# Kernel optimization log

Hardware: AMD Instinct MI355X
Metric: run time of the kernel (lower is better)

Reference implementation:

```python
import jax, jax.numpy as jnp
import numpy as np


def setup_inputs() -> dict:
    key = jax.random.key(0)
    k1, k2 = jax.random.split(key)
    user_attributes = jax.random.normal(k1, (32, 128, 256), dtype=jnp.float32)
    image_attributes = jax.random.normal(k2, (32, 256, 256), dtype=jnp.float32)
    return {"user_attributes": user_attributes, "image_attributes": image_attributes}


def reference(user_attributes, image_attributes):
    # Math: inter[b,u,i,d] = user[b,u,d] * img[b,i,d]
    #   sum over i -> user[b,u,d] * sum_i img[b,i,d]
    #   sum over u -> img[b,i,d]  * sum_u user[b,u,d]
    # Algebraically identical to the O(U*I*D) broadcast, without materializing it.
    img_sum = jnp.sum(image_attributes, axis=1, keepdims=True)   # [B,1,D]
    user_sum = jnp.sum(user_attributes, axis=1, keepdims=True)   # [B,1,D]
    aggregated_interactions_user = user_attributes * img_sum     # [B,U,D]
    aggregated_interactions_img = image_attributes * user_sum    # [B,I,D]
    return (aggregated_interactions_user, aggregated_interactions_img)
```

## Files before the change

kernel.cpp:

```cpp
#include <hip/hip_runtime.h>

#define B 32
#define U 128
#define I 256
#define D 256

#define PU_OFF 0
#define PI_OFF (B * 4 * D)

__global__ void __launch_bounds__(256) reduce_partial_kernel(
    const float* __restrict__ user,
    const float* __restrict__ img,
    float* __restrict__ ws) {
  __shared__ float4 part[4][64];
  const int blk  = blockIdx.x;
  const int tid  = threadIdx.x;
  const int rg   = tid >> 6;
  const int lane = tid & 63;

  const float4* src4;
  float4* dst4;
  if (blk < 128) {
    const int b = blk >> 2, c = blk & 3;
    src4 = (const float4*)(user + (size_t)b * U * D) + (size_t)c * 32 * 64;
    dst4 = (float4*)(ws + PU_OFF) + (size_t)(b * 4 + c) * 64;
  } else {
    const int k = blk - 128;
    const int b = k >> 3, c = k & 7;
    src4 = (const float4*)(img + (size_t)b * I * D) + (size_t)c * 32 * 64;
    dst4 = (float4*)(ws + PI_OFF) + (size_t)(b * 8 + c) * 64;
  }

  float4 acc = make_float4(0.f, 0.f, 0.f, 0.f);
  #pragma unroll
  for (int it = 0; it < 8; ++it) {
    const float4 v = src4[(size_t)(rg * 8 + it) * 64 + lane];
    acc.x += v.x; acc.y += v.y; acc.z += v.z; acc.w += v.w;
  }
  part[rg][lane] = acc;
  __syncthreads();
  if (rg == 0) {
    const float4 a = part[0][lane];
    const float4 b4 = part[1][lane];
    const float4 c = part[2][lane];
    const float4 e = part[3][lane];
    dst4[lane] = make_float4(a.x + b4.x + c.x + e.x,
                             a.y + b4.y + c.y + e.y,
                             a.z + b4.z + c.z + e.z,
                             a.w + b4.w + c.w + e.w);
  }
}

__global__ void __launch_bounds__(256) multiply_kernel(
    const float* __restrict__ user,
    const float* __restrict__ img,
    const float* __restrict__ ws,
    float* __restrict__ out) {
  constexpr int U4  = U * D / 4;
  constexpr int I4  = I * D / 4;
  constexpr int NU4 = B * U4;
  constexpr int NI4 = B * I4;

  const int g = blockIdx.x * blockDim.x + threadIdx.x;
  const float4* u4  = (const float4*)user;
  const float4* i4  = (const float4*)img;
  const float4* pu4 = (const float4*)(ws + PU_OFF);
  const float4* pi4 = (const float4*)(ws + PI_OFF);
  float4* o4 = (float4*)out;

  if (g < NU4) {
    const int b  = g >> 13;
    const int d4 = g & 63;
    const float4* p = pi4 + (size_t)b * 8 * 64 + d4;
    float4 s = p[0];
    #pragma unroll
    for (int c = 1; c < 8; ++c) {
      const float4 t = p[(size_t)c * 64];
      s.x += t.x; s.y += t.y; s.z += t.z; s.w += t.w;
    }
    const float4 v = u4[g];
    o4[g] = make_float4(v.x * s.x, v.y * s.y, v.z * s.z, v.w * s.w);
  } else if (g < NU4 + NI4) {
    const int k  = g - NU4;
    const int b  = k >> 14;
    const int d4 = k & 63;
    const float4* p = pu4 + (size_t)b * 4 * 64 + d4;
    float4 s = p[0];
    #pragma unroll
    for (int c = 1; c < 4; ++c) {
      const float4 t = p[(size_t)c * 64];
      s.x += t.x; s.y += t.y; s.z += t.z; s.w += t.w;
    }
    const float4 v = i4[k];
    o4[NU4 + k] = make_float4(v.x * s.x, v.y * s.y, v.z * s.z, v.w * s.w);
  }
}

extern "C" void kernel_launch(void* const* d_in, const int* in_sizes, int n_in,
                              void* d_out, int out_size, void* d_ws, size_t ws_size,
                              hipStream_t stream) {
  const float* user = (const float*)d_in[0];
  const float* img  = (const float*)d_in[1];
  float* out = (float*)d_out;
  float* ws  = (float*)d_ws;

  reduce_partial_kernel<<<dim3(384), dim3(256), 0, stream>>>(user, img, ws);

  constexpr int total4 = (B * U * D + B * I * D) / 4;
  multiply_kernel<<<dim3(total4 / 256), dim3(256), 0, stream>>>(user, img, ws, out);
}
```

Measured before the change: 71.16 us.

## Fuse column-sum reduction and scaling into a single kernel with redundant reductions

Replaces the two-kernel pipeline (partial reductions to workspace, then an elementwise multiply) with one kernel. Each block recomputes the full column sum of the opposite tensor for its batch and then scales its own 32-row slice. This removes one launch, the workspace round trip and the dependency between kernels. The cost is redundant reads: each img batch is summed by 4 blocks and each user batch by 8, roughly doubling total input reads, though some of those may hit in cache.

```diff
diff --git a/kernel.cpp b/kernel.cpp
--- a/kernel.cpp
+++ b/kernel.cpp
@@ -4,95 +4,78 @@
 #define U 128
 #define I 256
 #define D 256
+#define D4 (D / 4)
 
-#define PU_OFF 0
-#define PI_OFF (B * 4 * D)
-
-__global__ void __launch_bounds__(256) reduce_partial_kernel(
+__global__ void __launch_bounds__(256) fused_interaction_kernel(
     const float* __restrict__ user,
     const float* __restrict__ img,
-    float* __restrict__ ws) {
+    float* __restrict__ out) {
   __shared__ float4 part[4][64];
-  const int blk  = blockIdx.x;
-  const int tid  = threadIdx.x;
-  const int rg   = tid >> 6;
-  const int lane = tid & 63;
+  const int tid = threadIdx.x;
+  const int rg  = tid >> 6;
+  const int d4  = tid & 63;
+  const int blk = blockIdx.x;
 
-  const float4* src4;
-  float4* dst4;
+  const float4* u4 = (const float4*)user;
+  const float4* i4 = (const float4*)img;
+  float4* o4 = (float4*)out;
+  constexpr size_t NU4 = (size_t)B * U * D4;
+
   if (blk < 128) {
     const int b = blk >> 2, c = blk & 3;
-    src4 = (const float4*)(user + (size_t)b * U * D) + (size_t)c * 32 * 64;
-    dst4 = (float4*)(ws + PU_OFF) + (size_t)(b * 4 + c) * 64;
+    const float4* ib = i4 + (size_t)b * I * D4;
+
+    float4 acc = make_float4(0.f, 0.f, 0.f, 0.f);
+    #pragma unroll 8
+    for (int t = 0; t < 64; ++t) {
+      const float4 v = ib[(size_t)(rg + 4 * t) * D4 + d4];
+      acc.x += v.x; acc.y += v.y; acc.z += v.z; acc.w += v.w;
+    }
+    part[rg][d4] = acc;
+    __syncthreads();
+    const float4 s0 = part[0][d4], s1 = part[1][d4];
+    const float4 s2 = part[2][d4], s3 = part[3][d4];
+    const float4 s = make_float4(s0.x + s1.x + s2.x + s3.x,
+                                 s0.y + s1.y + s2.y + s3.y,
+                                 s0.z + s1.z + s2.z + s3.z,
+                                 s0.w + s1.w + s2.w + s3.w);
+
+    const float4* ub = u4 + (size_t)b * U * D4;
+    float4* ob = o4 + (size_t)b * U * D4;
+    #pragma unroll
+    for (int it = 0; it < 8; ++it) {
+      const size_t r = (size_t)(c * 32 + rg * 8 + it);
+      const float4 v = ub[r * D4 + d4];
+      ob[r * D4 + d4] = make_float4(v.x * s.x, v.y * s.y, v.z * s.z, v.w * s.w);
+    }
   } else {
     const int k = blk - 128;
     const int b = k >> 3, c = k & 7;
-    src4 = (const float4*)(img + (size_t)b * I * D) + (size_t)c * 32 * 64;
-    dst4 = (float4*)(ws + PI_OFF) + (size_t)(b * 8 + c) * 64;
-  }
+    const float4* ub = u4 + (size_t)b * U * D4;
 
-  float4 acc = make_float4(0.f, 0.f, 0.f, 0.f);
-  #pragma unroll
-  for (int it = 0; it < 8; ++it) {
-    const float4 v = src4[(size_t)(rg * 8 + it) * 64 + lane];
-    acc.x += v.x; acc.y += v.y; acc.z += v.z; acc.w += v.w;
-  }
-  part[rg][lane] = acc;
-  __syncthreads();
-  if (rg == 0) {
-    const float4 a = part[0][lane];
-    const float4 b4 = part[1][lane];
-    const float4 c = part[2][lane];
-    const float4 e = part[3][lane];
-    dst4[lane] = make_float4(a.x + b4.x + c.x + e.x,
-                             a.y + b4.y + c.y + e.y,
-                             a.z + b4.z + c.z + e.z,
-                             a.w + b4.w + c.w + e.w);
-  }
-}
+    float4 acc = make_float4(0.f, 0.f, 0.f, 0.f);
+    #pragma unroll 8
+    for (int t = 0; t < 32; ++t) {
+      const float4 v = ub[(size_t)(rg + 4 * t) * D4 + d4];
+      acc.x += v.x; acc.y += v.y; acc.z += v.z; acc.w += v.w;
+    }
+    part[rg][d4] = acc;
+    __syncthreads();
+    const float4 s0 = part[0][d4], s1 = part[1][d4];
+    const float4 s2 = part[2][d4], s3 = part[3][d4];
+    const float4 s = make_float4(s0.x + s1.x + s2.x + s3.x,
+                                 s0.y + s1.y + s2.y + s3.y,
+                                 s0.z + s1.z + s2.z + s3.z,
+                                 s0.w + s1.w + s2.w + s3.w);
 
-__global__ void __launch_bounds__(256) multiply_kernel(
-    const float* __restrict__ user,
-    const float* __restrict__ img,
-    const float* __restrict__ ws,
-    float* __restrict__ out) {
-  constexpr int U4  = U * D / 4;
-  constexpr int I4  = I * D / 4;
-  constexpr int NU4 = B * U4;
-  constexpr int NI4 = B * I4;
-
-  const int g = blockIdx.x * blockDim.x + threadIdx.x;
-  const float4* u4  = (const float4*)user;
-  const float4* i4  = (const float4*)img;
-  const float4* pu4 = (const float4*)(ws + PU_OFF);
-  const float4* pi4 = (const float4*)(ws + PI_OFF);
-  float4* o4 = (float4*)out;
-
-  if (g < NU4) {
-    const int b  = g >> 13;
-    const int d4 = g & 63;
-    const float4* p = pi4 + (size_t)b * 8 * 64 + d4;
-    float4 s = p[0];
+    const float4* ib = i4 + (size_t)b * I * D4;
+    float4* ob = o4 + NU4 + (size_t)b * I * D4;
     #pragma unroll
-    for (int c = 1; c < 8; ++c) {
-      const float4 t = p[(size_t)c * 64];
-      s.x += t.x; s.y += t.y; s.z += t.z; s.w += t.w;
+    for (int it = 0; it < 8; ++it) {
+      const size_t r = (size_t)(c * 32 + rg * 8 + it);
+      const float4 v = ib[r * D4 + d4];
+      ob[r * D4 + d4] = make_float4(v.x * s.x, v.y * s.y, v.z * s.z, v.w * s.w);
     }
-    const float4 v = u4[g];
-    o4[g] = make_float4(v.x * s.x, v.y * s.y, v.z * s.z, v.w * s.w);
-  } else if (g < NU4 + NI4) {
-    const int k  = g - NU4;
-    const int b  = k >> 14;
-    const int d4 = k & 63;
-    const float4* p = pu4 + (size_t)b * 4 * 64 + d4;
-    float4 s = p[0];
-    #pragma unroll
-    for (int c = 1; c < 4; ++c) {
-      const float4 t = p[(size_t)c * 64];
-      s.x += t.x; s.y += t.y; s.z += t.z; s.w += t.w;
-    }
-    const float4 v = i4[k];
-    o4[NU4 + k] = make_float4(v.x * s.x, v.y * s.y, v.z * s.z, v.w * s.w);
   }
 }
 
@@ -102,10 +85,7 @@
   const float* user = (const float*)d_in[0];
   const float* img  = (const float*)d_in[1];
   float* out = (float*)d_out;
-  float* ws  = (float*)d_ws;
+  (void)d_ws; (void)ws_size;
 
-  reduce_partial_kernel<<<dim3(384), dim3(256), 0, stream>>>(user, img, ws);
-
-  constexpr int total4 = (B * U * D + B * I * D) / 4;
-  multiply_kernel<<<dim3(total4 / 256), dim3(256), 0, stream>>>(user, img, ws, out);
+  fused_interaction_kernel<<<dim3(384), dim3(256), 0, stream>>>(user, img, out);
 }
```

After: 74.31 us. 1.04x slower.
